# Optimization experiments

Hardware: AMD Instinct MI355X
Metric: run time of the kernel (lower is better)

Reference implementation:

```python
import jax, jax.numpy as jnp
import numpy as np

EPS = 1e-5  # torch BatchNorm2d default eps

# BinaryActivation with STE: grad zeroed where |x| >= 1 (the extra 1.3 clip in
# xnor_binarize.backward is a subset and thus redundant).
@jax.custom_vjp
def sign_act(x):
    return jnp.sign(x)

def _sa_fwd(x):
    return jnp.sign(x), x

def _sa_bwd(x, g):
    mask = ((x > -1.0) & (x < 1.0)).astype(g.dtype)
    return (g * mask,)

sign_act.defvjp(_sa_fwd, _sa_bwd)

# Weight binarization (scale=False path): w.data.clamp_(-1,1) then sign();
# backward is straight-through identity (|bi_weight|=1 < 1.3 so clip never fires).
@jax.custom_vjp
def bin_weight(w):
    return jnp.sign(jnp.clip(w, -1.0, 1.0))

def _bw_fwd(w):
    return jnp.sign(jnp.clip(w, -1.0, 1.0)), None

def _bw_bwd(_, g):
    return (g,)

bin_weight.defvjp(_bw_fwd, _bw_bwd)


def _branch(x, gamma, beta, w, bias):
    # BatchNorm2d (training-mode batch stats, biased var), affine
    mu = jnp.mean(x, axis=(0, 2, 3), keepdims=True)
    var = jnp.var(x, axis=(0, 2, 3), keepdims=True)
    h = (x - mu) * jax.lax.rsqrt(var + EPS)
    h = h * gamma[None, :, None, None] + beta[None, :, None, None]
    # XNOR conv: binarized activations and weights, stride 2, pad 1
    a = sign_act(h)
    bw = bin_weight(w)
    y = jax.lax.conv_general_dilated(
        a, bw, window_strides=(2, 2), padding=[(1, 1), (1, 1)],
        dimension_numbers=('NCHW', 'OIHW', 'NCHW'))
    y = y + bias[None, :, None, None]
    # shortcut: AvgPool2d(kernel_size=2) (stride defaults to 2)
    B, C, H, W = x.shape
    sc = x.reshape(B, C, H // 2, 2, W // 2, 2).mean(axis=(3, 5))
    return jax.nn.relu(y) + sc


def setup_inputs() -> dict:
    key = jax.random.key(0)
    ks = jax.random.split(key, 9)
    B, C, H, W = 32, 192, 64, 64
    K = 3
    x = jax.random.normal(ks[0], (B, C, H, W), dtype=jnp.float32)
    g1 = 1.0 + 0.1 * jax.random.normal(ks[1], (C,), dtype=jnp.float32)
    b1 = 0.1 * jax.random.normal(ks[2], (C,), dtype=jnp.float32)
    w1 = 0.05 * jax.random.normal(ks[3], (C, C, K, K), dtype=jnp.float32)
    bias1 = jnp.zeros((C,), dtype=jnp.float32)
    g2 = 1.0 + 0.1 * jax.random.normal(ks[4], (C,), dtype=jnp.float32)
    b2 = 0.1 * jax.random.normal(ks[5], (C,), dtype=jnp.float32)
    w2 = 0.05 * jax.random.normal(ks[6], (C, C, K, K), dtype=jnp.float32)
    bias2 = jnp.zeros((C,), dtype=jnp.float32)
    return {"x": x, "g1": g1, "b1": b1, "w1": w1, "bias1": bias1,
            "g2": g2, "b2": b2, "w2": w2, "bias2": bias2}


def reference(x, g1, b1, w1, bias1, g2, b2, w2, bias2):
    x1 = _branch(x, g1, b1, w1, bias1)
    x2 = _branch(x, g2, b2, w2, bias2)
    return jnp.concatenate([x1, x2], axis=1)  # [B, 2C, H/2, W/2]
```

## Files before the change

### kernel.cpp

```cpp
#include <hip/hip_runtime.h>
#include <hip/hip_bf16.h>

typedef unsigned int u32;

#define BN 32
#define CC 192
#define HH 64
#define WW 64
#define HWSZ (HH*WW)
#define OHH 32
#define OWW 32
#define NVALID_SCALE 131072.0f
#define PLW 65
#define PLSZ (PLW*PLW)
#define NPLANE (12*BN)

__global__ __launch_bounds__(256) void k_stats(const float* __restrict__ x,
                                               float* __restrict__ partial) {
    int b = blockIdx.x;
    int c = b >> 5, n = b & 31;
    const float4* p = (const float4*)(x + ((size_t)(n * CC + c) << 12));
    int tid = threadIdx.x;
    float s = 0.f, s2 = 0.f;
#pragma unroll
    for (int k = 0; k < 4; ++k) {
        float4 f = p[tid + 256 * k];
        s  += f.x + f.y + f.z + f.w;
        s2 += f.x * f.x + f.y * f.y + f.z * f.z + f.w * f.w;
    }
#pragma unroll
    for (int off = 32; off > 0; off >>= 1) {
        s  += __shfl_down(s, off, 64);
        s2 += __shfl_down(s2, off, 64);
    }
    __shared__ float red[8];
    int wv = tid >> 6, ln = tid & 63;
    if (ln == 0) { red[wv * 2] = s; red[wv * 2 + 1] = s2; }
    __syncthreads();
    if (tid == 0) {
        partial[b * 2]     = red[0] + red[2] + red[4] + red[6];
        partial[b * 2 + 1] = red[1] + red[3] + red[5] + red[7];
    }
}

__global__ __launch_bounds__(64) void k_coef(const float* __restrict__ partial,
        const float* __restrict__ g1, const float* __restrict__ b1,
        const float* __restrict__ g2, const float* __restrict__ b2,
        float* __restrict__ coef) {
    int c = blockIdx.x;
    int t = threadIdx.x;
    int half = t >> 5, i = t & 31;
    float v = partial[(c * 32 + i) * 2 + half];
#pragma unroll
    for (int off = 16; off > 0; off >>= 1) v += __shfl_down(v, off, 32);
    float S2 = __shfl(v, 32, 64);
    if (t == 0) {
        float S = v;
        const float inv = 1.0f / NVALID_SCALE;
        float mu  = S * inv;
        float var = S2 * inv - mu * mu;
        float r   = 1.0f / sqrtf(var + 1e-5f);
        float s1 = g1[c] * r, t1 = b1[c] - mu * s1;
        float s2 = g2[c] * r, t2 = b2[c] - mu * s2;
        ((float4*)coef)[c] = make_float4(s1, t1, s2, t2);
    }
}

__global__ __launch_bounds__(256) void k_pack_w(const float* __restrict__ w1,
        const float* __restrict__ w2, u32* __restrict__ wp, u32* __restrict__ wsum) {
    __shared__ float wl[CC * 9];
    __shared__ u32 ww[54];
    int b  = blockIdx.x;
    int br = b / CC, oc = b - br * CC;
    const float* W = (br ? w2 : w1) + (size_t)oc * CC * 9;
    int tid = threadIdx.x;
    for (int i = tid; i < CC * 9; i += 256) wl[i] = W[i];
    __syncthreads();
    if (tid < 54) {
        int w6 = tid % 6, pos = tid / 6;
        u32 word = 0;
#pragma unroll
        for (int bb = 0; bb < 32; ++bb) {
            if (wl[(w6 * 32 + bb) * 9 + pos] > 0.f) word |= (1u << bb);
        }
        wp[(size_t)b * 54 + tid] = word;
        ww[tid] = word;
    }
    __syncthreads();
    if (tid == 0) {
        int Wt[9];
#pragma unroll
        for (int t = 0; t < 9; ++t) {
            int s = 0;
#pragma unroll
            for (int w6 = 0; w6 < 6; ++w6) s += __popc(ww[t * 6 + w6]);
            Wt[t] = s;
        }
        wsum[b * 4 + 0] = (u32)(Wt[0] + Wt[1] + Wt[2]);
        wsum[b * 4 + 1] = (u32)(Wt[0] + Wt[3] + Wt[6]);
        wsum[b * 4 + 2] = (u32)Wt[0];
        wsum[b * 4 + 3] = 0;
    }
}

__global__ __launch_bounds__(192) void k_halo(u32* __restrict__ act) {
    u32* pl = act + (size_t)blockIdx.x * PLSZ;
    int t = threadIdx.x;
    if (t < PLW) pl[t] = 0;
    else if (t < 2 * PLW - 1) pl[(t - PLW + 1) * PLW] = 0;
}

__global__ __launch_bounds__(256) void k_pack_act(const float* __restrict__ x,
        const float* __restrict__ coef, u32* __restrict__ act) {
    int tile = blockIdx.x;
    int g    = blockIdx.y;
    int n = tile >> 4, pxt = tile & 15;
    int px = pxt * 256 + threadIdx.x;
    int h = px >> 6, w = px & 63;
    const float*  xb = x + (size_t)n * CC * HWSZ + px;
    const float4* c4 = (const float4*)coef;
    u32 pk1 = 0, pk2 = 0;
#pragma unroll 8
    for (int bb = 0; bb < 32; ++bb) {
        int ch = g * 32 + bb;
        float v = xb[(size_t)ch * HWSZ];
        float4 cf = c4[ch];
        u32 bit = 1u << bb;
        if (v * cf.x + cf.y > 0.f) pk1 |= bit;
        if (v * cf.z + cf.w > 0.f) pk2 |= bit;
    }
    size_t off = (size_t)(h + 1) * PLW + (w + 1);
    act[((size_t)(0 * 6 + g) * BN + n) * PLSZ + off] = pk1;
    act[((size_t)(1 * 6 + g) * BN + n) * PLSZ + off] = pk2;
}

__global__ __launch_bounds__(256) void k_conv(
        const u32* __restrict__ act, const u32* __restrict__ wp,
        const u32* __restrict__ wsum, const float* __restrict__ x,
        const float* __restrict__ bias1, const float* __restrict__ bias2,
        float* __restrict__ out) {
    int b    = blockIdx.x;
    int tile = b >> 2;
    int n    = tile >> 4, ohp = tile & 15;
    int wid  = __builtin_amdgcn_readfirstlane((int)(threadIdx.x >> 6));
    int ocbase = ((b & 3) * 4 + wid) * 12;
    int lane = threadIdx.x & 63;
    int ow = lane & 31, lh = lane >> 5;
    int oh = 2 * ohp + lh;
    int lbase = (2 * oh) * PLW + 2 * ow;
    int topE  = (oh == 0), leftE = (ow == 0);
    int nv192 = CC * ((topE ? 2 : 3) * (leftE ? 2 : 3));
    float sc[12];
#pragma unroll 1
    for (int br = 0; br < 2; ++br) {
        u32 a[54];
        const u32* ap = act + ((size_t)(br * 6) * BN + n) * PLSZ + lbase;
#pragma unroll
        for (int w6 = 0; w6 < 6; ++w6) {
            const u32* app = ap + (size_t)w6 * (BN * PLSZ);
#pragma unroll
            for (int t = 0; t < 9; ++t) {
                a[t * 6 + w6] = app[(t / 3) * PLW + (t % 3)];
            }
        }
        const u32*   wqb = wp   + (size_t)(br * CC + ocbase) * 54;
        const u32*   wsb = wsum + (size_t)(br * CC + ocbase) * 4;
        const float* bsp = (br ? bias2 : bias1) + ocbase;
#pragma unroll 2
        for (int j = 0; j < 12; ++j) {
            u32 wv[54];
#pragma unroll
            for (int k = 0; k < 54; ++k) wv[k] = wqb[j * 54 + k];
            int p = 0;
#pragma unroll
            for (int k = 0; k < 54; ++k) p += __popc(a[k] ^ wv[k]);
            int Wr = (int)wsb[j * 4], Wc = (int)wsb[j * 4 + 1], Wk = (int)wsb[j * 4 + 2];
            int corr = (topE ? Wr : 0) + (leftE ? Wc : 0) - ((topE & leftE) ? Wk : 0);
            int dot = nv192 - 2 * p + 2 * corr;
            int oc = ocbase + j;
            float y = (float)dot + bsp[j];
            if (br == 0) {
                const float* xp = x + (((size_t)n * CC + oc) * HH + 2 * oh) * WW + 2 * ow;
                float2 r0 = *(const float2*)xp;
                float2 r1 = *(const float2*)(xp + WW);
                sc[j] = (r0.x + r0.y + r1.x + r1.y) * 0.25f;
            }
            out[((size_t)(n * 384 + br * CC + oc) * OHH + oh) * OWW + ow] =
                fmaxf(y, 0.f) + sc[j];
        }
    }
}

extern "C" void kernel_launch(void* const* d_in, const int* in_sizes, int n_in,
                              void* d_out, int out_size, void* d_ws, size_t ws_size,
                              hipStream_t stream) {
    const float* x     = (const float*)d_in[0];
    const float* g1    = (const float*)d_in[1];
    const float* b1    = (const float*)d_in[2];
    const float* w1    = (const float*)d_in[3];
    const float* bias1 = (const float*)d_in[4];
    const float* g2    = (const float*)d_in[5];
    const float* b2    = (const float*)d_in[6];
    const float* w2    = (const float*)d_in[7];
    const float* bias2 = (const float*)d_in[8];
    float* out = (float*)d_out;
    char* ws = (char*)d_ws;
    float* partial = (float*)(ws);
    float* coef    = (float*)(ws + 49152);
    u32*   wp      = (u32*)  (ws + 52224);
    u32*   wsum    = (u32*)  (ws + 135168);
    u32*   act     = (u32*)  (ws + 141312);

    hipLaunchKernelGGL(k_stats,    dim3(CC * BN),      dim3(256), 0, stream, x, partial);
    hipLaunchKernelGGL(k_coef,     dim3(CC),           dim3(64),  0, stream, partial, g1, b1, g2, b2, coef);
    hipLaunchKernelGGL(k_pack_w,   dim3(2 * CC),       dim3(256), 0, stream, w1, w2, wp, wsum);
    hipLaunchKernelGGL(k_halo,     dim3(NPLANE),       dim3(192), 0, stream, act);
    hipLaunchKernelGGL(k_pack_act, dim3(512, 6),       dim3(256), 0, stream, x, coef, act);
    hipLaunchKernelGGL(k_conv,     dim3(BN * 16 * 4),  dim3(256), 0, stream, act, wp, wsum, x, bias1, bias2, out);
}
```

Baseline: 245.4 us.

## Fuse stats, weight pack and halo into one front kernel; precompute avgpool shortcut

Merges the stats, weight-packing and halo-zeroing kernels into a single launch, removing two launch boundaries. The activation packer now handles 2x2 pixel quads per thread and computes the avg-pool shortcut into a workspace buffer, which the conv kernel reads instead of re-reading x. Plane rows are padded to 66 words so each quad writes aligned uint2 pairs. Output stores become nontemporal. In exchange, an extra 25 MB shortcut buffer is written and read back.

```diff
diff --git a/kernel.cpp b/kernel.cpp
--- a/kernel.cpp
+++ b/kernel.cpp
@@ -1,5 +1,4 @@
 #include <hip/hip_runtime.h>
-#include <hip/hip_bf16.h>
 
 typedef unsigned int u32;
 
@@ -11,35 +10,81 @@
 #define OHH 32
 #define OWW 32
 #define NVALID_SCALE 131072.0f
-#define PLW 65
-#define PLSZ (PLW*PLW)
+#define PLH 65
+#define PLW2 66
+#define PLSZ (PLH*PLW2)
 #define NPLANE (12*BN)
-
-__global__ __launch_bounds__(256) void k_stats(const float* __restrict__ x,
-                                               float* __restrict__ partial) {
-    int b = blockIdx.x;
-    int c = b >> 5, n = b & 31;
-    const float4* p = (const float4*)(x + ((size_t)(n * CC + c) << 12));
+#define NSTATS (CC*BN)
+#define NPW (2*CC)
+
+__global__ __launch_bounds__(256) void k_front(const float* __restrict__ x,
+        float* __restrict__ partial,
+        const float* __restrict__ w1, const float* __restrict__ w2,
+        u32* __restrict__ wp, u32* __restrict__ wsum,
+        u32* __restrict__ act) {
+    __shared__ float red[8];
+    __shared__ float wl[CC * 9];
+    __shared__ u32 ww[54];
+    int blk = blockIdx.x;
     int tid = threadIdx.x;
-    float s = 0.f, s2 = 0.f;
-#pragma unroll
-    for (int k = 0; k < 4; ++k) {
-        float4 f = p[tid + 256 * k];
-        s  += f.x + f.y + f.z + f.w;
-        s2 += f.x * f.x + f.y * f.y + f.z * f.z + f.w * f.w;
-    }
-#pragma unroll
-    for (int off = 32; off > 0; off >>= 1) {
-        s  += __shfl_down(s, off, 64);
-        s2 += __shfl_down(s2, off, 64);
-    }
-    __shared__ float red[8];
-    int wv = tid >> 6, ln = tid & 63;
-    if (ln == 0) { red[wv * 2] = s; red[wv * 2 + 1] = s2; }
-    __syncthreads();
-    if (tid == 0) {
-        partial[b * 2]     = red[0] + red[2] + red[4] + red[6];
-        partial[b * 2 + 1] = red[1] + red[3] + red[5] + red[7];
+    if (blk < NSTATS) {
+        int c = blk >> 5, n = blk & 31;
+        const float4* p = (const float4*)(x + ((size_t)(n * CC + c) << 12));
+        float s = 0.f, s2 = 0.f;
+#pragma unroll
+        for (int k = 0; k < 4; ++k) {
+            float4 f = p[tid + 256 * k];
+            s  += f.x + f.y + f.z + f.w;
+            s2 += f.x * f.x + f.y * f.y + f.z * f.z + f.w * f.w;
+        }
+#pragma unroll
+        for (int off = 32; off > 0; off >>= 1) {
+            s  += __shfl_down(s, off, 64);
+            s2 += __shfl_down(s2, off, 64);
+        }
+        int wv = tid >> 6, ln = tid & 63;
+        if (ln == 0) { red[wv * 2] = s; red[wv * 2 + 1] = s2; }
+        __syncthreads();
+        if (tid == 0) {
+            partial[blk * 2]     = red[0] + red[2] + red[4] + red[6];
+            partial[blk * 2 + 1] = red[1] + red[3] + red[5] + red[7];
+        }
+    } else if (blk < NSTATS + NPW) {
+        int b  = blk - NSTATS;
+        int br = b / CC, oc = b - br * CC;
+        const float* W = (br ? w2 : w1) + (size_t)oc * CC * 9;
+        for (int i = tid; i < CC * 9; i += 256) wl[i] = W[i];
+        __syncthreads();
+        if (tid < 54) {
+            int w6 = tid % 6, pos = tid / 6;
+            u32 word = 0;
+#pragma unroll
+            for (int bb = 0; bb < 32; ++bb) {
+                if (wl[(w6 * 32 + bb) * 9 + pos] > 0.f) word |= (1u << bb);
+            }
+            wp[(size_t)b * 54 + tid] = word;
+            ww[tid] = word;
+        }
+        __syncthreads();
+        if (tid == 0) {
+            int Wt[9];
+#pragma unroll
+            for (int t = 0; t < 9; ++t) {
+                int s = 0;
+#pragma unroll
+                for (int w6 = 0; w6 < 6; ++w6) s += __popc(ww[t * 6 + w6]);
+                Wt[t] = s;
+            }
+            wsum[b * 4 + 0] = (u32)(Wt[0] + Wt[1] + Wt[2]);
+            wsum[b * 4 + 1] = (u32)(Wt[0] + Wt[3] + Wt[6]);
+            wsum[b * 4 + 2] = (u32)Wt[0];
+            wsum[b * 4 + 3] = 0;
+        }
+    } else {
+        int plane = blk - NSTATS - NPW;
+        u32* pl = act + (size_t)plane * PLSZ;
+        if (tid < PLW2) pl[tid] = 0;
+        else if (tid < PLW2 + 64) pl[(tid - PLW2 + 1) * PLW2 + 1] = 0;
     }
 }
 
@@ -66,77 +111,48 @@
     }
 }
 
-__global__ __launch_bounds__(256) void k_pack_w(const float* __restrict__ w1,
-        const float* __restrict__ w2, u32* __restrict__ wp, u32* __restrict__ wsum) {
-    __shared__ float wl[CC * 9];
-    __shared__ u32 ww[54];
-    int b  = blockIdx.x;
-    int br = b / CC, oc = b - br * CC;
-    const float* W = (br ? w2 : w1) + (size_t)oc * CC * 9;
+__global__ __launch_bounds__(256) void k_pack_act(const float* __restrict__ x,
+        const float* __restrict__ coef, u32* __restrict__ act,
+        float* __restrict__ scb) {
+    int bx = blockIdx.x;
+    int g  = blockIdx.y;
+    int n = bx >> 2, q = bx & 3;
     int tid = threadIdx.x;
-    for (int i = tid; i < CC * 9; i += 256) wl[i] = W[i];
-    __syncthreads();
-    if (tid < 54) {
-        int w6 = tid % 6, pos = tid / 6;
-        u32 word = 0;
-#pragma unroll
-        for (int bb = 0; bb < 32; ++bb) {
-            if (wl[(w6 * 32 + bb) * 9 + pos] > 0.f) word |= (1u << bb);
-        }
-        wp[(size_t)b * 54 + tid] = word;
-        ww[tid] = word;
-    }
-    __syncthreads();
-    if (tid == 0) {
-        int Wt[9];
-#pragma unroll
-        for (int t = 0; t < 9; ++t) {
-            int s = 0;
-#pragma unroll
-            for (int w6 = 0; w6 < 6; ++w6) s += __popc(ww[t * 6 + w6]);
-            Wt[t] = s;
-        }
-        wsum[b * 4 + 0] = (u32)(Wt[0] + Wt[1] + Wt[2]);
-        wsum[b * 4 + 1] = (u32)(Wt[0] + Wt[3] + Wt[6]);
-        wsum[b * 4 + 2] = (u32)Wt[0];
-        wsum[b * 4 + 3] = 0;
-    }
-}
-
-__global__ __launch_bounds__(192) void k_halo(u32* __restrict__ act) {
-    u32* pl = act + (size_t)blockIdx.x * PLSZ;
-    int t = threadIdx.x;
-    if (t < PLW) pl[t] = 0;
-    else if (t < 2 * PLW - 1) pl[(t - PLW + 1) * PLW] = 0;
-}
-
-__global__ __launch_bounds__(256) void k_pack_act(const float* __restrict__ x,
-        const float* __restrict__ coef, u32* __restrict__ act) {
-    int tile = blockIdx.x;
-    int g    = blockIdx.y;
-    int n = tile >> 4, pxt = tile & 15;
-    int px = pxt * 256 + threadIdx.x;
-    int h = px >> 6, w = px & 63;
-    const float*  xb = x + (size_t)n * CC * HWSZ + px;
+    int ow = tid & 31, oh = (q << 3) + (tid >> 5);
     const float4* c4 = (const float4*)coef;
-    u32 pk1 = 0, pk2 = 0;
-#pragma unroll 8
+    const float* xb = x + (size_t)n * CC * HWSZ + (size_t)(2 * oh) * WW + 2 * ow;
+    float* scp = scb + ((size_t)(n * CC + g * 32) * OHH + oh) * OWW + ow;
+    u32 pk[8] = {0, 0, 0, 0, 0, 0, 0, 0};
+#pragma unroll 4
     for (int bb = 0; bb < 32; ++bb) {
         int ch = g * 32 + bb;
-        float v = xb[(size_t)ch * HWSZ];
+        const float* p = xb + (size_t)ch * HWSZ;
+        float2 r0 = *(const float2*)p;
+        float2 r1 = *(const float2*)(p + WW);
+        scp[(size_t)bb * (OHH * OWW)] = (r0.x + r0.y + r1.x + r1.y) * 0.25f;
         float4 cf = c4[ch];
         u32 bit = 1u << bb;
-        if (v * cf.x + cf.y > 0.f) pk1 |= bit;
-        if (v * cf.z + cf.w > 0.f) pk2 |= bit;
-    }
-    size_t off = (size_t)(h + 1) * PLW + (w + 1);
-    act[((size_t)(0 * 6 + g) * BN + n) * PLSZ + off] = pk1;
-    act[((size_t)(1 * 6 + g) * BN + n) * PLSZ + off] = pk2;
+        if (r0.x * cf.x + cf.y > 0.f) pk[0] |= bit;
+        if (r0.y * cf.x + cf.y > 0.f) pk[1] |= bit;
+        if (r1.x * cf.x + cf.y > 0.f) pk[2] |= bit;
+        if (r1.y * cf.x + cf.y > 0.f) pk[3] |= bit;
+        if (r0.x * cf.z + cf.w > 0.f) pk[4] |= bit;
+        if (r0.y * cf.z + cf.w > 0.f) pk[5] |= bit;
+        if (r1.x * cf.z + cf.w > 0.f) pk[6] |= bit;
+        if (r1.y * cf.z + cf.w > 0.f) pk[7] |= bit;
+    }
+    size_t o00 = (size_t)(2 * oh + 1) * PLW2 + (2 * ow + 2);
+    u32* a1 = act + ((size_t)(0 * 6 + g) * BN + n) * PLSZ + o00;
+    u32* a2 = act + ((size_t)(1 * 6 + g) * BN + n) * PLSZ + o00;
+    *(uint2*)a1            = make_uint2(pk[0], pk[1]);
+    *(uint2*)(a1 + PLW2)   = make_uint2(pk[2], pk[3]);
+    *(uint2*)a2            = make_uint2(pk[4], pk[5]);
+    *(uint2*)(a2 + PLW2)   = make_uint2(pk[6], pk[7]);
 }
 
 __global__ __launch_bounds__(256) void k_conv(
         const u32* __restrict__ act, const u32* __restrict__ wp,
-        const u32* __restrict__ wsum, const float* __restrict__ x,
+        const u32* __restrict__ wsum, const float* __restrict__ scb,
         const float* __restrict__ bias1, const float* __restrict__ bias2,
         float* __restrict__ out) {
     int b    = blockIdx.x;
@@ -147,7 +163,7 @@
     int lane = threadIdx.x & 63;
     int ow = lane & 31, lh = lane >> 5;
     int oh = 2 * ohp + lh;
-    int lbase = (2 * oh) * PLW + 2 * ow;
+    int lbase = (2 * oh) * PLW2 + 2 * ow + 1;
     int topE  = (oh == 0), leftE = (ow == 0);
     int nv192 = CC * ((topE ? 2 : 3) * (leftE ? 2 : 3));
     float sc[12];
@@ -160,7 +176,7 @@
             const u32* app = ap + (size_t)w6 * (BN * PLSZ);
 #pragma unroll
             for (int t = 0; t < 9; ++t) {
-                a[t * 6 + w6] = app[(t / 3) * PLW + (t % 3)];
+                a[t * 6 + w6] = app[(t / 3) * PLW2 + (t % 3)];
             }
         }
         const u32*   wqb = wp   + (size_t)(br * CC + ocbase) * 54;
@@ -180,13 +196,10 @@
             int oc = ocbase + j;
             float y = (float)dot + bsp[j];
             if (br == 0) {
-                const float* xp = x + (((size_t)n * CC + oc) * HH + 2 * oh) * WW + 2 * ow;
-                float2 r0 = *(const float2*)xp;
-                float2 r1 = *(const float2*)(xp + WW);
-                sc[j] = (r0.x + r0.y + r1.x + r1.y) * 0.25f;
-            }
-            out[((size_t)(n * 384 + br * CC + oc) * OHH + oh) * OWW + ow] =
-                fmaxf(y, 0.f) + sc[j];
+                sc[j] = scb[((size_t)(n * CC + oc) * OHH + oh) * OWW + ow];
+            }
+            __builtin_nontemporal_store(fmaxf(y, 0.f) + sc[j],
+                &out[((size_t)(n * 384 + br * CC + oc) * OHH + oh) * OWW + ow]);
         }
     }
 }
@@ -209,12 +222,15 @@
     float* coef    = (float*)(ws + 49152);
     u32*   wp      = (u32*)  (ws + 52224);
     u32*   wsum    = (u32*)  (ws + 135168);
-    u32*   act     = (u32*)  (ws + 141312);
-
-    hipLaunchKernelGGL(k_stats,    dim3(CC * BN),      dim3(256), 0, stream, x, partial);
-    hipLaunchKernelGGL(k_coef,     dim3(CC),           dim3(64),  0, stream, partial, g1, b1, g2, b2, coef);
-    hipLaunchKernelGGL(k_pack_w,   dim3(2 * CC),       dim3(256), 0, stream, w1, w2, wp, wsum);
-    hipLaunchKernelGGL(k_halo,     dim3(NPLANE),       dim3(192), 0, stream, act);
-    hipLaunchKernelGGL(k_pack_act, dim3(512, 6),       dim3(256), 0, stream, x, coef, act);
-    hipLaunchKernelGGL(k_conv,     dim3(BN * 16 * 4),  dim3(256), 0, stream, act, wp, wsum, x, bias1, bias2, out);
-}
+    float* scb     = (float*)(ws + 141312);
+    u32*   act     = (u32*)  (ws + 25307136);
+
+    hipLaunchKernelGGL(k_front,   dim3(NSTATS + NPW + NPLANE), dim3(256), 0, stream,
+                       x, partial, w1, w2, wp, wsum, act);
+    hipLaunchKernelGGL(k_coef,    dim3(CC),          dim3(64),  0, stream,
+                       partial, g1, b1, g2, b2, coef);
+    hipLaunchKernelGGL(k_pack_act, dim3(128, 6),     dim3(256), 0, stream,
+                       x, coef, act, scb);
+    hipLaunchKernelGGL(k_conv,    dim3(BN * 16 * 4), dim3(256), 0, stream,
+                       act, wp, wsum, scb, bias1, bias2, out);
+}
```

Measured after the change: 243.2 us. No clear change (-0.9%).
